# Kernel tuning notes

Measured on AMD Instinct MI355X. Metric: run time of the kernel, lower is better.

Reference implementation:

```python
import jax, jax.numpy as jnp
import numpy as np

N, F, H, L, O, E = 20000, 128, 128, 4, 64, 640000
NEG_SLOPE = 0.2  # PyG GATConv default


def setup_inputs() -> dict:
    key = jax.random.key(0)
    ks = jax.random.split(key, 8)
    x = jax.random.normal(ks[0], (N, F), dtype=jnp.float32)
    edge_index = jax.random.randint(ks[1], (2, E), 0, N, dtype=jnp.int64)
    sc = 1.0 / np.sqrt(F)
    Ws = jax.random.normal(ks[2], (L, F, H), dtype=jnp.float32) * sc
    att_src = jax.random.normal(ks[3], (L, H), dtype=jnp.float32) * sc
    att_dst = jax.random.normal(ks[4], (L, H), dtype=jnp.float32) * sc
    biases = jnp.zeros((L, H), dtype=jnp.float32)
    W_out = jax.random.normal(ks[5], (H, O), dtype=jnp.float32) * (1.0 / np.sqrt(H))
    b_out = jnp.zeros((O,), dtype=jnp.float32)
    return {"x": x, "edge_index": edge_index, "Ws": Ws, "att_src": att_src,
            "att_dst": att_dst, "biases": biases, "W_out": W_out, "b_out": b_out}


def _gat_conv(h, src, dst, W, a_s, a_d, b):
    # h: [N, F_in]; single-head GATConv (PyG semantics)
    z = h @ W                                   # [N, H]
    alpha_s = z @ a_s                           # [N]
    alpha_d = z @ a_d                           # [N]
    logits = jax.nn.leaky_relu(alpha_s[src] + alpha_d[dst], negative_slope=NEG_SLOPE)  # [E']
    # segment-softmax over edges grouped by destination node
    m = jax.ops.segment_max(logits, dst, num_segments=N)
    p = jnp.exp(logits - m[dst])
    s = jax.ops.segment_sum(p, dst, num_segments=N)
    alpha = p / (s[dst] + 1e-16)                # [E']
    out = jax.ops.segment_sum(alpha[:, None] * z[src], dst, num_segments=N)  # [N, H]
    return out + b


def reference(x, edge_index, Ws, att_src, att_dst, biases, W_out, b_out):
    # add self-loops once (PyG GATConv default add_self_loops=True)
    loop = jnp.arange(N, dtype=edge_index.dtype)
    src = jnp.concatenate([edge_index[0], loop])
    dst = jnp.concatenate([edge_index[1], loop])
    h = x
    for l in range(L):
        h = _gat_conv(h, src, dst, Ws[l], att_src[l], att_dst[l], biases[l])
        h = jax.nn.relu(h)  # Dropout is identity at eval
    return h @ W_out + b_out  # [N, O]
```

## Files before the change

kernel.cpp:

```cpp
#include <hip/hip_runtime.h>

#define NN 20000
#define FF 128
#define HH 128
#define LL 4
#define OO 64
#define EE 640000
#define NEG 0.2f
#define NB ((NN + 255) / 256)

typedef short bf16x8 __attribute__((ext_vector_type(8)));
typedef float f32x4 __attribute__((ext_vector_type(4)));

__device__ inline ushort f2bf(float f) {
    uint u = __float_as_uint(f);
    return (ushort)((u + 0x7fffu + ((u >> 16) & 1u)) >> 16);
}


__global__ void k_init_counters(int* __restrict__ counters) {
    int i = blockIdx.x * 256 + threadIdx.x;
    if (i < NN) counters[i] = 1;
}

__global__ void k_hist(const int* __restrict__ dst, int* __restrict__ counters) {
    int e = blockIdx.x * 256 + threadIdx.x;
    if (e < EE) atomicAdd(&counters[dst[e]], 1);
}

__global__ void k_partial(const int* __restrict__ counters, int* __restrict__ partials) {
    __shared__ int ws[4];
    int t = threadIdx.x;
    int i = blockIdx.x * 256 + t;
    int c = (i < NN) ? counters[i] : 0;
    #pragma unroll
    for (int off = 32; off; off >>= 1) c += __shfl_xor(c, off);
    if ((t & 63) == 0) ws[t >> 6] = c;
    __syncthreads();
    if (t == 0) partials[blockIdx.x] = ws[0] + ws[1] + ws[2] + ws[3];
}

__global__ void k_scan_small(const int* __restrict__ partials, int* __restrict__ offsets) {
    __shared__ int sp[128];
    int t = threadIdx.x;
    int v = (t < NB) ? partials[t] : 0;
    sp[t] = v;
    __syncthreads();
    for (int off = 1; off < 128; off <<= 1) {
        int u = (t >= off) ? sp[t - off] : 0;
        __syncthreads();
        sp[t] += u;
        __syncthreads();
    }
    if (t < NB) offsets[t] = sp[t] - v;
}

__global__ void k_apply(const int* __restrict__ counters, const int* __restrict__ offsets,
                        int* __restrict__ row_off, int* __restrict__ cursor,
                        int* __restrict__ src_sorted) {
    __shared__ int sc[256];
    int t = threadIdx.x;
    int i = blockIdx.x * 256 + t;
    int c = (i < NN) ? counters[i] : 0;
    sc[t] = c;
    __syncthreads();
    for (int off = 1; off < 256; off <<= 1) {
        int u = (t >= off) ? sc[t - off] : 0;
        __syncthreads();
        sc[t] += u;
        __syncthreads();
    }
    int incl = sc[t];
    int base = offsets[blockIdx.x];
    if (i < NN) {
        int excl = base + incl - c;
        row_off[i] = excl;
        cursor[i] = excl + 1;
        src_sorted[excl] = i;
        if (i == NN - 1) row_off[NN] = base + incl;
    }
}

__global__ void k_scatter(const int* __restrict__ src, const int* __restrict__ dst,
                          int* __restrict__ cursor, int* __restrict__ src_sorted) {
    int e = blockIdx.x * 256 + threadIdx.x;
    if (e < EE) {
        int p = atomicAdd(&cursor[dst[e]], 1);
        src_sorted[p] = src[e];
    }
}


__global__ void k_convw(const float* __restrict__ Ws, const float* __restrict__ Wout,
                        ushort* __restrict__ wh, ushort* __restrict__ wl) {
    int idx = blockIdx.x * 256 + threadIdx.x;
    const int per_l = HH * 128;
    float v;
    if (idx < LL * per_l) {
        int l = idx / per_l, rem = idx % per_l;
        int n = rem >> 7, k = rem & 127;
        v = Ws[(size_t)l * 128 * HH + (size_t)k * HH + n];
    } else {
        int j = idx - LL * per_l;
        if (j >= OO * 128) return;
        int n = j >> 7, k = j & 127;
        v = Wout[(size_t)k * OO + n];
    }
    ushort h = f2bf(v);
    float hf = __uint_as_float((uint)h << 16);
    wh[idx] = h;
    wl[idx] = f2bf(v - hf);
}


template <int NCOL, bool BIAS, bool ALPHAS>
__global__ void k_gemm_mfma(const float* __restrict__ A, const ushort* __restrict__ wh,
                            const ushort* __restrict__ wl, const float* __restrict__ bias,
                            float* __restrict__ C,
                            const float* __restrict__ a_s, const float* __restrict__ a_d,
                            float* __restrict__ as_out, float* __restrict__ ad_out) {
    constexpr int NT = NCOL / 16;
    int l = threadIdx.x;
    int row0 = blockIdx.x * 16;
    int lr = l & 15, lg = l >> 4;

    const float* arow = A + (size_t)(row0 + lr) * 128;
    f32x4 af0[4], af1[4];
    #pragma unroll
    for (int s = 0; s < 4; s++) {
        af0[s] = *(const f32x4*)(arow + s * 32 + lg * 8);
        af1[s] = *(const f32x4*)(arow + s * 32 + lg * 8 + 4);
    }
    bf16x8 ah[4], al[4];
    #pragma unroll
    for (int s = 0; s < 4; s++) {
        #pragma unroll
        for (int j = 0; j < 8; j++) {
            float v = (j < 4) ? af0[s][j] : af1[s][j - 4];
            ushort h = f2bf(v);
            float hf = __uint_as_float((uint)h << 16);
            ah[s][j] = (short)h;
            al[s][j] = (short)f2bf(v - hf);
        }
    }

    f32x4 acc[NT];
    #pragma unroll
    for (int nt = 0; nt < NT; nt++) acc[nt] = (f32x4){0.f, 0.f, 0.f, 0.f};

    #pragma unroll
    for (int s = 0; s < 4; s++) {
        #pragma unroll
        for (int nt = 0; nt < NT; nt++) {
            int woff = (nt * 16 + lr) * 128 + s * 32 + lg * 8;
            bf16x8 bh = *(const bf16x8*)(wh + woff);
            bf16x8 bl = *(const bf16x8*)(wl + woff);
            acc[nt] = __builtin_amdgcn_mfma_f32_16x16x32_bf16(ah[s], bh, acc[nt], 0, 0, 0);
            acc[nt] = __builtin_amdgcn_mfma_f32_16x16x32_bf16(ah[s], bl, acc[nt], 0, 0, 0);
            acc[nt] = __builtin_amdgcn_mfma_f32_16x16x32_bf16(al[s], bh, acc[nt], 0, 0, 0);
        }
    }

    int orow = lg * 4;
    #pragma unroll
    for (int nt = 0; nt < NT; nt++) {
        #pragma unroll
        for (int r = 0; r < 4; r++) {
            float v = acc[nt][r];
            if (BIAS) v += bias[nt * 16 + lr];
            C[(size_t)(row0 + orow + r) * NCOL + nt * 16 + lr] = v;
        }
    }

    if constexpr (ALPHAS) {
        #pragma unroll
        for (int r = 0; r < 4; r++) {
            float ps = 0.f, pd = 0.f;
            #pragma unroll
            for (int nt = 0; nt < NT; nt++) {
                ps += acc[nt][r] * a_s[nt * 16 + lr];
                pd += acc[nt][r] * a_d[nt * 16 + lr];
            }
            #pragma unroll
            for (int off = 1; off < 16; off <<= 1) {
                ps += __shfl_xor(ps, off);
                pd += __shfl_xor(pd, off);
            }
            if (lr == 0) {
                as_out[row0 + orow + r] = ps;
                ad_out[row0 + orow + r] = pd;
            }
        }
    }
}


__global__ void k_aggregate(const float* __restrict__ z, const float* __restrict__ as,
                            const float* __restrict__ ad, const int* __restrict__ row_off,
                            const int* __restrict__ srcs, const float* __restrict__ bias,
                            float* __restrict__ out) {
    int node = blockIdx.x * 4 + (threadIdx.x >> 6);
    int lane = threadIdx.x & 63;
    if (node >= NN) return;
    int beg = row_off[node], end = row_off[node + 1];
    float adn = ad[node];
    float lself = as[node] + adn;
    float mx = (lself >= 0.f) ? lself : NEG * lself;

    int g = lane >> 5, cl = lane & 31;
    const float4* zb = (const float4*)z;
    float4 acc = make_float4(0.f, 0.f, 0.f, 0.f);
    float s = 0.f;

    for (int e = beg + g; e < end; e += 16) {
        int e1 = e + 2, e2 = e + 4, e3 = e + 6, e4 = e + 8, e5 = e + 10, e6 = e + 12, e7 = e + 14;
        int lim = end - 1;
        int i1 = min(e1, lim), i2 = min(e2, lim), i3 = min(e3, lim);
        int i4 = min(e4, lim), i5 = min(e5, lim), i6 = min(e6, lim), i7 = min(e7, lim);
        int s0 = srcs[e], s1 = srcs[i1], s2 = srcs[i2], s3 = srcs[i3];
        int s4 = srcs[i4], s5 = srcs[i5], s6 = srcs[i6], s7 = srcs[i7];
        float l0 = as[s0] + adn, l1 = as[s1] + adn, l2 = as[s2] + adn, l3 = as[s3] + adn;
        float l4 = as[s4] + adn, l5 = as[s5] + adn, l6 = as[s6] + adn, l7 = as[s7] + adn;
        l0 = (l0 >= 0.f) ? l0 : NEG * l0;  l1 = (l1 >= 0.f) ? l1 : NEG * l1;
        l2 = (l2 >= 0.f) ? l2 : NEG * l2;  l3 = (l3 >= 0.f) ? l3 : NEG * l3;
        l4 = (l4 >= 0.f) ? l4 : NEG * l4;  l5 = (l5 >= 0.f) ? l5 : NEG * l5;
        l6 = (l6 >= 0.f) ? l6 : NEG * l6;  l7 = (l7 >= 0.f) ? l7 : NEG * l7;
        float4 z0 = zb[(size_t)s0 * 32 + cl];
        float4 z1 = zb[(size_t)s1 * 32 + cl];
        float4 z2 = zb[(size_t)s2 * 32 + cl];
        float4 z3 = zb[(size_t)s3 * 32 + cl];
        float4 z4 = zb[(size_t)s4 * 32 + cl];
        float4 z5 = zb[(size_t)s5 * 32 + cl];
        float4 z6 = zb[(size_t)s6 * 32 + cl];
        float4 z7 = zb[(size_t)s7 * 32 + cl];
        float p0 = __expf(l0 - mx);
        float p1 = (e1 < end) ? __expf(l1 - mx) : 0.f;
        float p2 = (e2 < end) ? __expf(l2 - mx) : 0.f;
        float p3 = (e3 < end) ? __expf(l3 - mx) : 0.f;
        float p4 = (e4 < end) ? __expf(l4 - mx) : 0.f;
        float p5 = (e5 < end) ? __expf(l5 - mx) : 0.f;
        float p6 = (e6 < end) ? __expf(l6 - mx) : 0.f;
        float p7 = (e7 < end) ? __expf(l7 - mx) : 0.f;
        s += ((p0 + p1) + (p2 + p3)) + ((p4 + p5) + (p6 + p7));
        acc.x += (p0 * z0.x + p1 * z1.x + p2 * z2.x + p3 * z3.x)
               + (p4 * z4.x + p5 * z5.x + p6 * z6.x + p7 * z7.x);
        acc.y += (p0 * z0.y + p1 * z1.y + p2 * z2.y + p3 * z3.y)
               + (p4 * z4.y + p5 * z5.y + p6 * z6.y + p7 * z7.y);
        acc.z += (p0 * z0.z + p1 * z1.z + p2 * z2.z + p3 * z3.z)
               + (p4 * z4.z + p5 * z5.z + p6 * z6.z + p7 * z7.z);
        acc.w += (p0 * z0.w + p1 * z1.w + p2 * z2.w + p3 * z3.w)
               + (p4 * z4.w + p5 * z5.w + p6 * z6.w + p7 * z7.w);
    }

    acc.x += __shfl_xor(acc.x, 32);
    acc.y += __shfl_xor(acc.y, 32);
    acc.z += __shfl_xor(acc.z, 32);
    acc.w += __shfl_xor(acc.w, 32);
    s     += __shfl_xor(s, 32);

    if (g == 0) {
        float inv = 1.f / (s + 1e-16f);
        float4 b = ((const float4*)bias)[cl];
        float4 o;
        o.x = fmaxf(acc.x * inv + b.x, 0.f);
        o.y = fmaxf(acc.y * inv + b.y, 0.f);
        o.z = fmaxf(acc.z * inv + b.z, 0.f);
        o.w = fmaxf(acc.w * inv + b.w, 0.f);
        ((float4*)out)[(size_t)node * 32 + cl] = o;
    }
}


extern "C" void kernel_launch(void* const* d_in, const int* in_sizes, int n_in,
                              void* d_out, int out_size, void* d_ws, size_t ws_size,
                              hipStream_t stream) {
    const float* x      = (const float*)d_in[0];
    const int*   ei     = (const int*)d_in[1];
    const float* Ws     = (const float*)d_in[2];
    const float* attS   = (const float*)d_in[3];
    const float* attD   = (const float*)d_in[4];
    const float* biases = (const float*)d_in[5];
    const float* W_out  = (const float*)d_in[6];
    const float* b_out  = (const float*)d_in[7];
    float* out = (float*)d_out;

    const int* srcp = ei;
    const int* dstp = ei + EE;

    char* w = (char*)d_ws;
    auto take = [&](size_t bytes) {
        char* p = w;
        w += (bytes + 15) & ~(size_t)15;
        return p;
    };
    float*  zbuf       = (float*)take((size_t)NN * HH * 4);
    float*  hbuf       = (float*)take((size_t)NN * HH * 4);
    float*  as_v       = (float*)take((size_t)NN * 4);
    float*  ad_v       = (float*)take((size_t)NN * 4);
    int*    counters   = (int*)take((size_t)NN * 4);
    int*    row_off    = (int*)take((size_t)(NN + 1) * 4);
    int*    cursor     = (int*)take((size_t)NN * 4);
    int*    src_sorted = (int*)take((size_t)(EE + NN) * 4);
    int*    partials   = (int*)take((size_t)NB * 4);
    int*    offsets    = (int*)take((size_t)NB * 4);
    const int WTOT = LL * HH * 128 + OO * 128;
    ushort* whbuf      = (ushort*)take((size_t)WTOT * 2);
    ushort* wlbuf      = (ushort*)take((size_t)WTOT * 2);

    k_init_counters<<<(NN + 255) / 256, 256, 0, stream>>>(counters);
    k_hist<<<(EE + 255) / 256, 256, 0, stream>>>(dstp, counters);
    k_partial<<<NB, 256, 0, stream>>>(counters, partials);
    k_scan_small<<<1, 128, 0, stream>>>(partials, offsets);
    k_apply<<<NB, 256, 0, stream>>>(counters, offsets, row_off, cursor, src_sorted);
    k_scatter<<<(EE + 255) / 256, 256, 0, stream>>>(srcp, dstp, cursor, src_sorted);
    k_convw<<<(WTOT + 255) / 256, 256, 0, stream>>>(Ws, W_out, whbuf, wlbuf);

    const int gemm_blocks = NN / 16;
    const int node_blocks = (NN + 3) / 4;

    for (int l = 0; l < LL; l++) {
        const float* hin = (l == 0) ? x : hbuf;
        k_gemm_mfma<HH, false, true><<<gemm_blocks, 64, 0, stream>>>(
            hin, whbuf + (size_t)l * HH * 128, wlbuf + (size_t)l * HH * 128,
            nullptr, zbuf, attS + l * HH, attD + l * HH, as_v, ad_v);
        k_aggregate<<<node_blocks, 256, 0, stream>>>(zbuf, as_v, ad_v, row_off, src_sorted,
                                                     biases + l * HH, hbuf);
    }

    k_gemm_mfma<OO, true, false><<<gemm_blocks, 64, 0, stream>>>(
        hbuf, whbuf + (size_t)LL * HH * 128, wlbuf + (size_t)LL * HH * 128,
        b_out, out, nullptr, nullptr, nullptr, nullptr);
}
```

Measured before the change: 333.4 us.

## Split GEMM columns across blocks and precompute W·a for attention scores

The MFMA GEMM now gives each block a 16x32 output tile instead of a full 16-row strip, which multiplies the block count by four (two for the output layer). This raises parallelism for the small per-layer GEMMs. Because the per-node attention scores no longer live in one block's accumulators, a new setup kernel precomputes W·att_src and W·att_dst. The first column-tile block then computes alpha_s/alpha_d directly from the fp32 input row. The cost is redundant loading and bf16 splitting of the A rows in every column block, plus a small reassociation of the attention-score arithmetic.

```diff
diff --git a/kernel.cpp b/kernel.cpp
--- a/kernel.cpp
+++ b/kernel.cpp
@@ -113,15 +113,30 @@
 }
 
 
+__global__ void k_wa(const float* __restrict__ Ws, const float* __restrict__ attS,
+                     const float* __restrict__ attD, float* __restrict__ wa) {
+    int t = blockIdx.x * 256 + threadIdx.x;
+    if (t >= LL * 256) return;
+    int l = t >> 8, rem = t & 255, which = rem >> 7, k = rem & 127;
+    const float* wrow = Ws + (size_t)l * 128 * HH + (size_t)k * HH;
+    const float* av = (which ? attD : attS) + l * HH;
+    float s = 0.f;
+    #pragma unroll 4
+    for (int n = 0; n < HH; n++) s += wrow[n] * av[n];
+    wa[l * 256 + which * 128 + k] = s;
+}
+
+
 template <int NCOL, bool BIAS, bool ALPHAS>
 __global__ void k_gemm_mfma(const float* __restrict__ A, const ushort* __restrict__ wh,
                             const ushort* __restrict__ wl, const float* __restrict__ bias,
-                            float* __restrict__ C,
-                            const float* __restrict__ a_s, const float* __restrict__ a_d,
+                            float* __restrict__ C, const float* __restrict__ wa,
                             float* __restrict__ as_out, float* __restrict__ ad_out) {
-    constexpr int NT = NCOL / 16;
+    constexpr int CT = NCOL / 32;
+    int bid = blockIdx.x;
+    int rt = bid / CT, ct = bid % CT;
     int l = threadIdx.x;
-    int row0 = blockIdx.x * 16;
+    int row0 = rt * 16, col0 = ct * 32;
     int lr = l & 15, lg = l >> 4;
 
     const float* arow = A + (size_t)(row0 + lr) * 128;
@@ -144,15 +159,13 @@
         }
     }
 
-    f32x4 acc[NT];
-    #pragma unroll
-    for (int nt = 0; nt < NT; nt++) acc[nt] = (f32x4){0.f, 0.f, 0.f, 0.f};
+    f32x4 acc[2] = {{0.f, 0.f, 0.f, 0.f}, {0.f, 0.f, 0.f, 0.f}};
 
     #pragma unroll
     for (int s = 0; s < 4; s++) {
         #pragma unroll
-        for (int nt = 0; nt < NT; nt++) {
-            int woff = (nt * 16 + lr) * 128 + s * 32 + lg * 8;
+        for (int nt = 0; nt < 2; nt++) {
+            int woff = (col0 + nt * 16 + lr) * 128 + s * 32 + lg * 8;
             bf16x8 bh = *(const bf16x8*)(wh + woff);
             bf16x8 bl = *(const bf16x8*)(wl + woff);
             acc[nt] = __builtin_amdgcn_mfma_f32_16x16x32_bf16(ah[s], bh, acc[nt], 0, 0, 0);
@@ -163,32 +176,33 @@
 
     int orow = lg * 4;
     #pragma unroll
-    for (int nt = 0; nt < NT; nt++) {
+    for (int nt = 0; nt < 2; nt++) {
         #pragma unroll
         for (int r = 0; r < 4; r++) {
             float v = acc[nt][r];
-            if (BIAS) v += bias[nt * 16 + lr];
-            C[(size_t)(row0 + orow + r) * NCOL + nt * 16 + lr] = v;
+            if (BIAS) v += bias[col0 + nt * 16 + lr];
+            C[(size_t)(row0 + orow + r) * NCOL + col0 + nt * 16 + lr] = v;
         }
     }
 
     if constexpr (ALPHAS) {
-        #pragma unroll
-        for (int r = 0; r < 4; r++) {
+        if (ct == 0) {
             float ps = 0.f, pd = 0.f;
             #pragma unroll
-            for (int nt = 0; nt < NT; nt++) {
-                ps += acc[nt][r] * a_s[nt * 16 + lr];
-                pd += acc[nt][r] * a_d[nt * 16 + lr];
+            for (int s = 0; s < 4; s++) {
+                #pragma unroll
+                for (int j = 0; j < 8; j++) {
+                    float v = (j < 4) ? af0[s][j] : af1[s][j - 4];
+                    int k = s * 32 + lg * 8 + j;
+                    ps += v * wa[k];
+                    pd += v * wa[128 + k];
+                }
             }
-            #pragma unroll
-            for (int off = 1; off < 16; off <<= 1) {
-                ps += __shfl_xor(ps, off);
-                pd += __shfl_xor(pd, off);
-            }
-            if (lr == 0) {
-                as_out[row0 + orow + r] = ps;
-                ad_out[row0 + orow + r] = pd;
+            ps += __shfl_xor(ps, 16);  pd += __shfl_xor(pd, 16);
+            ps += __shfl_xor(ps, 32);  pd += __shfl_xor(pd, 32);
+            if (lg == 0) {
+                as_out[row0 + lr] = ps;
+                ad_out[row0 + lr] = pd;
             }
         }
     }
@@ -306,6 +320,7 @@
     const int WTOT = LL * HH * 128 + OO * 128;
     ushort* whbuf      = (ushort*)take((size_t)WTOT * 2);
     ushort* wlbuf      = (ushort*)take((size_t)WTOT * 2);
+    float*  wabuf      = (float*)take((size_t)LL * 256 * 4);
 
     k_init_counters<<<(NN + 255) / 256, 256, 0, stream>>>(counters);
     k_hist<<<(EE + 255) / 256, 256, 0, stream>>>(dstp, counters);
@@ -314,20 +329,20 @@
     k_apply<<<NB, 256, 0, stream>>>(counters, offsets, row_off, cursor, src_sorted);
     k_scatter<<<(EE + 255) / 256, 256, 0, stream>>>(srcp, dstp, cursor, src_sorted);
     k_convw<<<(WTOT + 255) / 256, 256, 0, stream>>>(Ws, W_out, whbuf, wlbuf);
-
-    const int gemm_blocks = NN / 16;
+    k_wa<<<(LL * 256 + 255) / 256, 256, 0, stream>>>(Ws, attS, attD, wabuf);
+
     const int node_blocks = (NN + 3) / 4;
 
     for (int l = 0; l < LL; l++) {
         const float* hin = (l == 0) ? x : hbuf;
-        k_gemm_mfma<HH, false, true><<<gemm_blocks, 64, 0, stream>>>(
+        k_gemm_mfma<HH, false, true><<<(NN / 16) * (HH / 32), 64, 0, stream>>>(
             hin, whbuf + (size_t)l * HH * 128, wlbuf + (size_t)l * HH * 128,
-            nullptr, zbuf, attS + l * HH, attD + l * HH, as_v, ad_v);
+            nullptr, zbuf, wabuf + l * 256, as_v, ad_v);
         k_aggregate<<<node_blocks, 256, 0, stream>>>(zbuf, as_v, ad_v, row_off, src_sorted,
                                                      biases + l * HH, hbuf);
     }
 
-    k_gemm_mfma<OO, true, false><<<gemm_blocks, 64, 0, stream>>>(
+    k_gemm_mfma<OO, true, false><<<(NN / 16) * (OO / 32), 64, 0, stream>>>(
         hbuf, whbuf + (size_t)LL * HH * 128, wlbuf + (size_t)LL * HH * 128,
-        b_out, out, nullptr, nullptr, nullptr, nullptr);
-}
+        b_out, out, nullptr, nullptr, nullptr);
+}
```

Result: no change. 329.9 us (-1.0%).
